# Performance work log

Measured on AMD Instinct MI355X. Metric: run time of the kernel, lower is better.

The kernel has to match this reference:

```python
import jax, jax.numpy as jnp
import numpy as np

N = 50000      # nodes
E = 800000     # edges (before self-loops)
NG = 64        # graphs
H, C = 4, 32   # heads, out channels per head
D = 128        # feature dim == H*C
GS, K = 4, 3   # grid_size, spline_order
NB = GS + K    # number of B-spline bases = 7
NC = 10        # classes
L = 3          # gnn layers

# uniform KAN grid over [-1,1] extended by spline_order on each side
GRID = jnp.arange(-K, GS + K + 1, dtype=jnp.float32) * (2.0 / GS) - 1.0  # [GS+2K+1]


def b_splines(x, grid, k):
    # x: [N, in] -> bases: [N, in, GS+k] via Cox-de Boor recursion
    xe = x[..., None]
    bases = ((xe >= grid[:-1]) & (xe < grid[1:])).astype(x.dtype)
    for p in range(1, k + 1):
        left = (xe - grid[:-(p + 1)]) / (grid[p:-1] - grid[:-(p + 1)]) * bases[..., :-1]
        right = (grid[p + 1:] - xe) / (grid[p + 1:] - grid[1:-p]) * bases[..., 1:]
        bases = left + right
    return bases


def kan_linear(x, base_w, spline_w, scaler):
    # efficient-kan: silu(x)@base_w.T + b_splines(x) contracted with scaled spline weights
    base = jax.nn.silu(x) @ base_w.T
    bs = b_splines(x, GRID, K)                      # [N, in, NB]
    sw = spline_w * scaler[..., None]               # [out, in, NB]
    return base + jnp.einsum('nib,oib->no', bs, sw)


def gat_layer(x, src, dst, base_w, spline_w, scaler, att_src, att_dst, bias):
    n = x.shape[0]
    h = kan_linear(x, base_w, spline_w, scaler).reshape(n, H, C)
    a_src = jnp.sum(h * att_src, axis=-1)           # [N, H]
    a_dst = jnp.sum(h * att_dst, axis=-1)           # [N, H]
    e = jax.nn.leaky_relu(a_src[src] + a_dst[dst], 0.2)  # [Etot, H]
    # segment softmax over incoming edges of each destination node
    m = jax.ops.segment_max(e, dst, num_segments=n)
    ex = jnp.exp(e - m[dst])
    s = jax.ops.segment_sum(ex, dst, num_segments=n)
    alpha = ex / (s[dst] + 1e-16)                   # [Etot, H]
    msg = h[src] * alpha[..., None]                 # [Etot, H, C]
    out = jax.ops.segment_sum(msg, dst, num_segments=n)
    return out.reshape(n, H * C) + bias


def setup_inputs() -> dict:
    key = jax.random.key(0)
    ks = jax.random.split(key, 16)
    inp = {
        'x': jax.random.normal(ks[0], (N, D), dtype=jnp.float32),
        'edge_index': jax.random.randint(ks[1], (2, E), 0, N, dtype=jnp.int32),
        'batch': jnp.sort(jax.random.randint(ks[2], (N,), 0, NG, dtype=jnp.int32)),
        # stacked per-layer GAT+KAN params (all layers are [128 -> 128])
        'base_w': jax.random.normal(ks[3], (L, D, D), dtype=jnp.float32) * 0.05,
        'spline_w': jax.random.normal(ks[4], (L, D, D, NB), dtype=jnp.float32) * 0.05,
        'scaler': jax.random.normal(ks[5], (L, D, D), dtype=jnp.float32) * 0.3 + 1.0,
        'att_src': jax.random.normal(ks[6], (L, H, C), dtype=jnp.float32) * 0.1,
        'att_dst': jax.random.normal(ks[7], (L, H, C), dtype=jnp.float32) * 0.1,
        'bias': jnp.zeros((L, H * C), dtype=jnp.float32),
        # readout KANLinear [128 -> 10]
        'ro_base_w': jax.random.normal(ks[8], (NC, D), dtype=jnp.float32) * 0.05,
        'ro_spline_w': jax.random.normal(ks[9], (NC, D, NB), dtype=jnp.float32) * 0.05,
        'ro_scaler': jax.random.normal(ks[10], (NC, D), dtype=jnp.float32) * 0.3 + 1.0,
    }
    return inp


def reference(x, edge_index, batch, base_w, spline_w, scaler, att_src, att_dst, bias,
              ro_base_w, ro_spline_w, ro_scaler):
    # PyG GATConv default: add self-loops
    loops = jnp.arange(N, dtype=edge_index.dtype)
    src = jnp.concatenate([edge_index[0], loops])
    dst = jnp.concatenate([edge_index[1], loops])
    h = x
    for i in range(L):
        h = gat_layer(h, src, dst, base_w[i], spline_w[i], scaler[i],
                      att_src[i], att_dst[i], bias[i])
        h = jax.nn.silu(h)  # dropout is identity in eval mode
    pooled = jax.ops.segment_sum(h, batch, num_segments=NG)   # global_add_pool [NG, D]
    logits = kan_linear(pooled, ro_base_w, ro_spline_w, ro_scaler)
    return jax.nn.log_softmax(logits, axis=1)
```

## Files before the change

### kernel.cpp

```cpp
#include <hip/hip_runtime.h>
#include <math.h>

#define NN 50000
#define EE 800000
#define ETOT (EE + NN)
#define NGR 64
#define DD 128
#define NCL 10

#define NBUK 128
#define BNODES 391
#define P1CH 3321
#define P2CAP 8704

typedef __attribute__((ext_vector_type(16))) float float16_t;
typedef __attribute__((ext_vector_type(8)))  __bf16 bf16x8;

__device__ __forceinline__ float siluf(float x){ return x / (1.f + __expf(-x)); }

__device__ __forceinline__ unsigned f2bf(float f){
  union { float f; unsigned u; } v; v.f = f;
  unsigned r = v.u + 0x7fffu + ((v.u >> 16) & 1u);
  return (r >> 16) & 0xffffu;
}

__device__ __forceinline__ void kan_feats(float x, float* f8){
  f8[0] = siluf(x);
  float u = 2.f*x + 5.f;
  int cell = -1;
  float n0=0.f,n1=0.f,n2=0.f,n3=0.f;
  if (u >= 0.f && u < 10.f){
    cell = (int)u;
    float t = u - (float)cell;
    float t2 = t*t, t3 = t2*t;
    float omt = 1.f - t;
    const float s6 = 1.f/6.f;
    n0 = t3*s6;
    n1 = s6*(1.f + 3.f*t + 3.f*t2 - 3.f*t3);
    n2 = s6*(4.f - 6.f*t2 + 3.f*t3);
    n3 = omt*omt*omt*s6;
  }
#pragma unroll
  for (int j=0;j<7;++j){
    int k = cell - j;
    float v = (k==0)?n0:((k==1)?n1:((k==2)?n2:((k==3)?n3:0.f)));
    f8[1+j] = v;
  }
}

__device__ __forceinline__ int4 kan_feats_pack(float x){
  unsigned sbf = f2bf(siluf(x));
  float u = 2.f*x + 5.f;
  bool valid = (u >= 0.f) && (u < 10.f);
  float uc = valid ? u : 0.f;
  int cell = (int)uc;
  float t = uc - (float)cell;
  float t2 = t*t, t3 = t2*t, omt = 1.f - t;
  const float s6 = 1.f/6.f;
  float n0 = t3*s6;
  float n1 = s6*(1.f + 3.f*t + 3.f*t2 - 3.f*t3);
  float n2 = s6*(4.f - 6.f*t2 + 3.f*t3);
  float n3 = omt*omt*omt*s6;
  unsigned p0=f2bf(n0), p1=f2bf(n1), p2=f2bf(n2), p3=f2bf(n3);
  unsigned long long P = ((unsigned long long)(p1 | (p0<<16)) << 32)
                       |  (unsigned long long)(p3 | (p2<<16));
  int sh = cell*16 - 48;
  unsigned long long shl    = P << (sh & 63);
  unsigned long long shrhi  = P >> ((64 - sh) & 63);
  unsigned long long shllo2 = P << ((sh - 64) & 63);
  unsigned long long shrlo  = P >> ((-sh) & 63);
  unsigned long long F0, F1;
  if (sh < 0)       { F0 = shrlo; F1 = 0ull; }
  else if (sh < 64) { F0 = shl;   F1 = (sh==0)? 0ull : shrhi; }
  else              { F0 = 0ull;  F1 = shllo2; }
  if (!valid){ F0 = 0ull; F1 = 0ull; }
  unsigned w0 = ((unsigned)(F0 & 0xffffull) << 16) | sbf;
  unsigned w1 = (unsigned)((F0 >> 16) & 0xffffffffull);
  unsigned w2 = (unsigned)((F0 >> 48) & 0xffffull) | (((unsigned)(F1 & 0xffffull)) << 16);
  unsigned w3 = (unsigned)((F1 >> 16) & 0xffffffffull);
  return make_int4((int)w0,(int)w1,(int)w2,(int)w3);
}

__global__ void hist_kernel(const int* __restrict__ ei, int* __restrict__ deg){
  int e = blockIdx.x*256 + threadIdx.x;
  if (e >= ETOT) return;
  int dst = (e < EE) ? ei[EE + e] : (e - EE);
  atomicAdd(&deg[dst], 1);
}

__global__ void scan1_kernel(const int* __restrict__ deg, int* __restrict__ offs, int* __restrict__ part){
  __shared__ int sh[256];
  int tid = threadIdx.x;
  int i = blockIdx.x*256 + tid;
  int v = (i < NN) ? deg[i] : 0;
  sh[tid] = v; __syncthreads();
  for (int o=1;o<256;o<<=1){
    int t2 = (tid >= o) ? sh[tid - o] : 0;
    __syncthreads();
    sh[tid] += t2;
    __syncthreads();
  }
  int incl = sh[tid];
  if (i < NN) offs[i] = incl - v;
  if (tid == 255) part[blockIdx.x] = incl;
}

__global__ void scan2_kernel(int* __restrict__ part, int nb){
  __shared__ int sh[256];
  int tid = threadIdx.x;
  int v = (tid < nb) ? part[tid] : 0;
  sh[tid] = v; __syncthreads();
  for (int o=1;o<256;o<<=1){
    int t2 = (tid >= o) ? sh[tid - o] : 0;
    __syncthreads();
    sh[tid] += t2;
    __syncthreads();
  }
  if (tid < nb) part[tid] = sh[tid] - v;
}

__global__ void scan3_kernel(int* __restrict__ offs, const int* __restrict__ part, int* __restrict__ cursor){
  int i = blockIdx.x*256 + threadIdx.x;
  if (i >= NN) return;
  int o = offs[i] + part[blockIdx.x];
  offs[i] = o;
  cursor[i] = o;
}

__global__ void binit_kernel(const int* __restrict__ offs, int* __restrict__ bcur){
  int b = threadIdx.x;
  if (b < NBUK) bcur[b] = offs[b*BNODES];
}

__global__ __launch_bounds__(256) void binpass_kernel(const int* __restrict__ ei,
                                                      int* __restrict__ bcur,
                                                      unsigned* __restrict__ tmp){
  __shared__ int cnt[NBUK], lexcl[NBUK], gbase[NBUK], lcur[NBUK];
  __shared__ int sc[NBUK];
  __shared__ unsigned entries[P1CH + 7];
  const int t = threadIdx.x;
  const int e0 = blockIdx.x * P1CH;
  int e1 = e0 + P1CH; if (e1 > ETOT) e1 = ETOT;
  const int total = e1 - e0;

  if (t < NBUK){ cnt[t] = 0; lcur[t] = 0; }
  __syncthreads();

  unsigned myE[14]; int myB[14]; int myN = 0;
  for (int e = e0 + t; e < e1; e += 256){
    int src, dst;
    if (e < EE){ src = ei[e]; dst = ei[EE + e]; } else { src = e - EE; dst = src; }
    int b = dst / BNODES;
    int dl = dst - b*BNODES;
    myE[myN] = ((unsigned)b << 25) | ((unsigned)dl << 16) | (unsigned)src;
    myB[myN] = b;
    myN++;
    atomicAdd(&cnt[b], 1);
  }
  __syncthreads();

  if (t < NBUK) sc[t] = cnt[t];
  __syncthreads();
  for (int o=1;o<NBUK;o<<=1){
    int v = 0;
    if (t < NBUK && t >= o) v = sc[t - o];
    __syncthreads();
    if (t < NBUK) sc[t] += v;
    __syncthreads();
  }
  if (t < NBUK) lexcl[t] = sc[t] - cnt[t];
  __syncthreads();

  if (t < NBUK && cnt[t] > 0) gbase[t] = atomicAdd(&bcur[t], cnt[t]);
  __syncthreads();

  for (int k=0;k<myN;++k){
    int b = myB[k];
    int r = lexcl[b] + atomicAdd(&lcur[b], 1);
    entries[r] = myE[k];
  }
  __syncthreads();

  for (int s = t; s < total; s += 256){
    unsigned en = entries[s];
    int b = en >> 25;
    int pos = gbase[b] + (s - lexcl[b]);
    tmp[pos] = en;
  }
}

__global__ __launch_bounds__(256) void scatter_kernel(const unsigned* __restrict__ tmp,
                                                      const int* __restrict__ offs,
                                                      int* __restrict__ cursor,
                                                      int* __restrict__ csr){
  __shared__ unsigned ebuf[P2CAP];
  __shared__ unsigned sbuf[P2CAP];
  __shared__ int dcnt[BNODES+1], dscan[BNODES+1], dcur[BNODES+1];
  __shared__ int sA[512], sB[512];
  const int t = threadIdx.x;
  const int b = blockIdx.x;
  const int lo = b * BNODES;
  const int start = offs[lo];
  const int end = (b < NBUK-1) ? offs[lo + BNODES] : ETOT;
  const int cnt = end - start;

  if (cnt > P2CAP){
    for (int i = t; i < cnt; i += 256){
      unsigned en = tmp[start + i];
      int node = lo + (int)((en >> 16) & 0x1FF);
      int pos = atomicAdd(&cursor[node], 1);
      csr[pos] = (int)(en & 0xFFFF);
    }
    return;
  }

  for (int i = t; i < cnt; i += 256) ebuf[i] = tmp[start + i];
  for (int i = t; i < BNODES+1; i += 256){ dcnt[i] = 0; dcur[i] = 0; }
  __syncthreads();
  for (int i = t; i < cnt; i += 256){
    int dl = (ebuf[i] >> 16) & 0x1FF;
    atomicAdd(&dcnt[dl], 1);
  }
  __syncthreads();

  sA[t]       = (t       < BNODES+1) ? dcnt[t]       : 0;
  sA[t + 256] = (t + 256 < BNODES+1) ? dcnt[t + 256] : 0;
  __syncthreads();
  int* sp = sA; int* dp = sB;
  for (int o=1;o<512;o<<=1){
    dp[t]       = sp[t]       + ((t       >= o) ? sp[t - o]       : 0);
    dp[t + 256] = sp[t + 256] + ((t + 256 >= o) ? sp[t + 256 - o] : 0);
    __syncthreads();
    int* tpp = sp; sp = dp; dp = tpp;
  }
  if (t       < BNODES+1) dscan[t]       = sp[t]       - dcnt[t];
  if (t + 256 < BNODES+1) dscan[t + 256] = sp[t + 256] - dcnt[t + 256];
  __syncthreads();

  for (int i = t; i < cnt; i += 256){
    unsigned en = ebuf[i];
    int dl = (en >> 16) & 0x1FF;
    int r = dscan[dl] + atomicAdd(&dcur[dl], 1);
    sbuf[r] = en & 0xFFFFu;
  }
  __syncthreads();
  for (int i = t; i < cnt; i += 256) csr[start + i] = (int)sbuf[i];
}

__global__ void build_wfrag(const float* __restrict__ bw, const float* __restrict__ sw,
                            const float* __restrict__ sc, unsigned short* __restrict__ wfrag){
  int idx = blockIdx.x*256 + threadIdx.x;
  if (idx >= 3*128*1024) return;
  int k = idx & 1023;
  int o = (idx >> 10) & 127;
  int l = idx >> 17;
  int i = k >> 3, f = k & 7;
  int oi = (l*DD + o)*DD + i;
  float w = (f == 0) ? bw[oi] : sw[oi*7 + (f-1)] * sc[oi];
  int s = k >> 6;
  int sl = (k >> 4) & 3, half = (k >> 3) & 1, j = k & 7;
  int ntile = o >> 5, n = o & 31;
  int dst = l*131072 + s*8192 + (((ntile*4 + sl)*64) + half*32 + n)*8 + j;
  wfrag[dst] = (unsigned short)f2bf(w);
}

__global__ __launch_bounds__(256, 5) void kan_gemm(const float* __restrict__ xin,
                                                const unsigned short* __restrict__ wfrag,
                                                const float* __restrict__ attS,
                                                const float* __restrict__ attD,
                                                unsigned int* __restrict__ hpack,
                                                float* __restrict__ asrc,
                                                float* __restrict__ adst, int layer)
{
  __shared__ __align__(16) unsigned short Afrag[2][4096];
  const int t    = threadIdx.x;
  const int lane = t & 63;
  const int w    = t >> 6;
  const int half = lane >> 5;
  const int mn   = lane & 31;
  const int row0 = blockIdx.x * 32;
  const unsigned short* wl = wfrag + layer*131072;

  const int m_my  = t & 31;
  const int il_my = t >> 5;
  const int grow_my = row0 + m_my;
  const float* xp = xin + (size_t)((grow_my < NN) ? grow_my : 0)*DD + il_my;
  const int fo = (il_my*32 + m_my)*8;

  float xv[16];
#pragma unroll
  for (int s=0;s<16;++s) xv[s] = xp[s*8];

  float16_t acc;
#pragma unroll
  for (int i=0;i<16;++i) acc[i]=0.f;

  int4 Bc[4], Bn[4];
#pragma unroll
  for (int sl=0;sl<4;++sl)
    Bc[sl] = *(const int4*)(wl + ((w*4+sl)*64 + lane)*8);

  *(int4*)(&Afrag[0][fo]) = kan_feats_pack(xv[0]);
  __syncthreads();

  for (int s=0; s<16; ++s){
    if (s < 15){
      const unsigned short* wsrc = wl + (s+1)*8192;
#pragma unroll
      for (int sl=0;sl<4;++sl)
        Bn[sl] = *(const int4*)(wsrc + ((w*4+sl)*64 + lane)*8);
      *(int4*)(&Afrag[(s+1)&1][fo]) = kan_feats_pack(xv[s+1]);
    }
    const unsigned short* A = Afrag[s&1];
#pragma unroll
    for (int sl=0; sl<4; ++sl){
      int4 ai = *(const int4*)(A + (((sl*2 + half)*32) + mn)*8);
      bf16x8 b = __builtin_bit_cast(bf16x8, Bc[sl]);
      acc = __builtin_amdgcn_mfma_f32_32x32x16_bf16(__builtin_bit_cast(bf16x8, ai), b, acc, 0, 0, 0);
    }
#pragma unroll
    for (int sl=0;sl<4;++sl) Bc[sl] = Bn[sl];
    __syncthreads();
  }

  unsigned short* hs = (unsigned short*)Afrag;
#pragma unroll
  for (int reg=0; reg<16; ++reg){
    int row = (reg&3) + 8*(reg>>2) + 4*half;
    hs[row*136 + w*32 + mn] = (unsigned short)f2bf(acc[reg]);
  }
  __syncthreads();
#pragma unroll
  for (int q=0;q<2;++q){
    int p = q*256 + t;
    int row = p >> 4, u4 = p & 15;
    uint4 v = *(const uint4*)((const unsigned int*)(hs + row*136) + u4*4);
    int grow = row0 + row;
    if (grow < NN) *(uint4*)(hpack + (size_t)grow*64 + u4*4) = v;
  }
  if (t < 128){
    int r = t >> 2, h = t & 3;
    const unsigned* hrow = (const unsigned*)(hs + r*136) + h*16;
    const float* ws = attS + (layer*4 + h)*32;
    const float* wd = attD + (layer*4 + h)*32;
    float ss = 0.f, sd = 0.f;
#pragma unroll
    for (int j=0;j<16;++j){
      int jj = (j + r) & 15;
      unsigned u = hrow[jj];
      float flo = __uint_as_float(u << 16);
      float fhi = __uint_as_float(u & 0xffff0000u);
      ss += flo*ws[2*jj] + fhi*ws[2*jj+1];
      sd += flo*wd[2*jj] + fhi*wd[2*jj+1];
    }
    int grow = row0 + r;
    if (grow < NN){ asrc[grow*4 + h] = ss; adst[grow*4 + h] = sd; }
  }
}

__global__ __launch_bounds__(256) void attn_kernel(
    const unsigned int* __restrict__ hpack, const float* __restrict__ asrc, const float* __restrict__ adst,
    const int* __restrict__ offs, const int* __restrict__ deg, const int* __restrict__ csr,
    const float* __restrict__ bias, float* __restrict__ hout, int layer)
{
  const int wave = threadIdx.x >> 6;
  const int lane = threadIdx.x & 63;
  const int n = blockIdx.x*4 + wave;
  if (n >= NN) return;
  const int st = offs[n];
  const int d  = deg[n];
  const int eL = lane >> 2, h = lane & 3;
  const float adh = adst[n*4 + h];

  int   srcv[4];
  float ev[4];
  float mL = -3.4e38f;
#pragma unroll
  for (int c=0;c<4;++c){
    srcv[c] = 0; ev[c] = -3.4e38f;
    int e = c*16 + eL;
    if (e < d){
      int s2 = csr[st + e];
      srcv[c] = s2;
      float e0 = asrc[s2*4 + h] + adh;
      ev[c] = (e0 > 0.f) ? e0 : 0.2f*e0;
      mL = fmaxf(mL, ev[c]);
    }
  }
  for (int c=64; c<d; c+=16){
    int e = c + eL;
    if (e < d){
      int s2 = csr[st + e];
      float e0 = asrc[s2*4 + h] + adh;
      float evv = (e0 > 0.f) ? e0 : 0.2f*e0;
      mL = fmaxf(mL, evv);
    }
  }
#pragma unroll
  for (int o=4;o<64;o<<=1) mL = fmaxf(mL, __shfl_xor(mL, o));

  float av4[4];
  float sL = 0.f;
#pragma unroll
  for (int c=0;c<4;++c){ av4[c] = __expf(ev[c] - mL); sL += av4[c]; }
  for (int c=64; c<d; c+=16){
    int e = c + eL;
    if (e < d){
      int s2 = csr[st + e];
      float e0 = asrc[s2*4 + h] + adh;
      float evv = (e0 > 0.f) ? e0 : 0.2f*e0;
      sL += __expf(evv - mL);
    }
  }
#pragma unroll
  for (int o=4;o<64;o<<=1) sL += __shfl_xor(sL, o);
  const float inv = 1.f/(sL + 1e-16f);

  const int hq = lane >> 4;
  float accL = 0.f, accH = 0.f;
#pragma unroll
  for (int c=0;c<4;++c){
    if (c*16 < d){
      float ac = av4[c] * inv;
      int lim = d - c*16; if (lim > 16) lim = 16;
      unsigned uv[16]; float aj[16];
#pragma unroll
      for (int j=0;j<16;++j){
        int sj = __shfl(srcv[c], j*4);
        aj[j]  = __shfl(ac,      j*4 + hq);
        if (j < lim) uv[j] = hpack[(size_t)sj*64 + lane];
        else         uv[j] = 0u;
      }
#pragma unroll
      for (int j=0;j<16;++j){
        accL = fmaf(aj[j], __uint_as_float(uv[j] << 16),         accL);
        accH = fmaf(aj[j], __uint_as_float(uv[j] & 0xffff0000u), accH);
      }
    }
  }
  for (int c=64; c<d; c+=16){
    int e = c + eL;
    int s2 = 0; float al = 0.f;
    if (e < d){
      s2 = csr[st + e];
      float e0 = asrc[s2*4 + h] + adh;
      float evv = (e0 > 0.f) ? e0 : 0.2f*e0;
      al = __expf(evv - mL) * inv;
    }
    int lim = d - c; if (lim > 16) lim = 16;
    for (int j=0;j<lim;++j){
      int sj = __shfl(s2, j*4);
      float aH = __shfl(al, j*4 + hq);
      unsigned u = hpack[(size_t)sj*64 + lane];
      accL = fmaf(aH, __uint_as_float(u << 16),         accL);
      accH = fmaf(aH, __uint_as_float(u & 0xffff0000u), accH);
    }
  }
  float2 bv = *(const float2*)(bias + layer*DD + 2*lane);
  float o0 = siluf(accL + bv.x);
  float o1 = siluf(accH + bv.y);
  *(float2*)(hout + (size_t)n*DD + 2*lane) = make_float2(o0, o1);
}

__global__ __launch_bounds__(128) void pool_kernel(const float* __restrict__ h,
    const int* __restrict__ batch, float* __restrict__ pooled)
{
  int c = threadIdx.x;
  int n0 = blockIdx.x*128;
  float sum = 0.f; int cur = -1;
  for (int r=0;r<128;++r){
    int n = n0 + r;
    if (n >= NN) break;
    int g = batch[n];
    if (g != cur){
      if (cur >= 0) atomicAdd(&pooled[cur*DD + c], sum);
      cur = g; sum = 0.f;
    }
    sum += h[n*DD + c];
  }
  if (cur >= 0) atomicAdd(&pooled[cur*DD + c], sum);
}

__global__ __launch_bounds__(64) void readout_kernel(const float* __restrict__ pooled,
    const float* __restrict__ bw, const float* __restrict__ sw, const float* __restrict__ sc,
    float* __restrict__ out)
{
  int g = blockIdx.x, lane = threadIdx.x;
  float xa = pooled[g*DD + lane];
  float xb = pooled[g*DD + lane + 64];
  float fa[8], fb[8];
  kan_feats(xa, fa);
  kan_feats(xb, fb);
  float logits[NCL];
#pragma unroll
  for (int c=0;c<NCL;++c){
    int ia = c*DD + lane, ib = ia + 64;
    float sca = sc[ia], scb = sc[ib];
    float p = fa[0]*bw[ia] + fb[0]*bw[ib];
#pragma unroll
    for (int f=1;f<8;++f)
      p += fa[f]*sw[ia*7 + f-1]*sca + fb[f]*sw[ib*7 + f-1]*scb;
#pragma unroll
    for (int o=1;o<64;o<<=1) p += __shfl_xor(p, o);
    logits[c] = p;
  }
  float mx = logits[0];
#pragma unroll
  for (int c=1;c<NCL;++c) mx = fmaxf(mx, logits[c]);
  float lse = 0.f;
#pragma unroll
  for (int c=0;c<NCL;++c) lse += __expf(logits[c]-mx);
  lse = mx + logf(lse);
  if (lane < NCL){
    float v = 0.f;
#pragma unroll
    for (int c=0;c<NCL;++c) if (lane == c) v = logits[c] - lse;
    out[g*NCL + lane] = v;
  }
}

extern "C" void kernel_launch(void* const* d_in, const int* in_sizes, int n_in,
                              void* d_out, int out_size, void* d_ws, size_t ws_size,
                              hipStream_t stream)
{
  const float* x        = (const float*)d_in[0];
  const int*   ei       = (const int*)  d_in[1];
  const int*   batch    = (const int*)  d_in[2];
  const float* base_w   = (const float*)d_in[3];
  const float* spline_w = (const float*)d_in[4];
  const float* scaler   = (const float*)d_in[5];
  const float* att_src  = (const float*)d_in[6];
  const float* att_dst  = (const float*)d_in[7];
  const float* bias     = (const float*)d_in[8];
  const float* ro_bw    = (const float*)d_in[9];
  const float* ro_sw    = (const float*)d_in[10];
  const float* ro_sc    = (const float*)d_in[11];
  float* out = (float*)d_out;

  char* p = (char*)d_ws;
  auto alloc = [&](size_t bytes)->char* {
    char* r = p;
    p += (bytes + 255) & ~(size_t)255;
    return r;
  };
  unsigned int* hpack = (unsigned int*)alloc((size_t)50048*64*4);
  float* hbuf   = (float*)alloc((size_t)NN*DD*4);
  unsigned short* wfrag = (unsigned short*)alloc((size_t)3*131072*2);
  float* asrc   = (float*)alloc((size_t)NN*4*4);
  float* adst   = (float*)alloc((size_t)NN*4*4);
  float* pooled = (float*)alloc((size_t)NGR*DD*4);
  int*   deg    = (int*)alloc((size_t)NN*4);
  int*   offs   = (int*)alloc((size_t)NN*4);
  int*   cursor = (int*)alloc((size_t)NN*4);
  int*   csr    = (int*)alloc((size_t)ETOT*4);
  unsigned* tmp = (unsigned*)alloc((size_t)ETOT*4);
  int*   bcur   = (int*)alloc((size_t)NBUK*4);
  int*   part   = (int*)alloc((size_t)256*4);

  const int nbs = (NN + 255)/256;
  hipMemsetAsync(deg, 0, (size_t)NN*sizeof(int), stream);
  hist_kernel   <<<(ETOT+255)/256, 256, 0, stream>>>(ei, deg);
  scan1_kernel  <<<nbs, 256, 0, stream>>>(deg, offs, part);
  scan2_kernel  <<<1,   256, 0, stream>>>(part, nbs);
  scan3_kernel  <<<nbs, 256, 0, stream>>>(offs, part, cursor);
  binit_kernel  <<<1,   128, 0, stream>>>(offs, bcur);
  binpass_kernel<<<256, 256, 0, stream>>>(ei, bcur, tmp);
  scatter_kernel<<<NBUK,256, 0, stream>>>(tmp, offs, cursor, csr);
  build_wfrag   <<<(3*128*1024)/256, 256, 0, stream>>>(base_w, spline_w, scaler, wfrag);

  const float* cur = x;
  for (int l=0; l<3; ++l){
    kan_gemm   <<<(NN+31)/32, 256, 0, stream>>>(cur, wfrag, att_src, att_dst,
                                                hpack, asrc, adst, l);
    attn_kernel<<<(NN+3)/4,   256, 0, stream>>>(hpack, asrc, adst, offs, deg, csr,
                                                bias, hbuf, l);
    cur = hbuf;
  }
  hipMemsetAsync(pooled, 0, (size_t)NGR*DD*sizeof(float), stream);
  pool_kernel   <<<(NN+127)/128, 128, 0, stream>>>(hbuf, batch, pooled);
  readout_kernel<<<NGR, 64, 0, stream>>>(pooled, ro_bw, ro_sw, ro_sc, out);
}
```

Before: 471.3 us.

## Restructure KAN GEMM so each wave computes a full 32x128 tile from registers

Each wave now owns 32 rows and computes all four 32-column output tiles. A operands are built directly in registers from x via kan_feats_pack, so the shared-memory A staging and the per-step block barriers go away. Blocks now cover 128 rows instead of 32. Weight fragments are read straight from global memory each step without register double-buffering, and the occupancy hint of 5 is dropped. The wave now holds 64 accumulator registers and needs more weight loads per wave, which trades barrier and LDS cost for register pressure and possible occupancy loss.

```diff
diff --git a/kernel.cpp b/kernel.cpp
--- a/kernel.cpp
+++ b/kernel.cpp
@@ -264,7 +264,7 @@
   wfrag[dst] = (unsigned short)f2bf(w);
 }
 
-__global__ __launch_bounds__(256, 5) void kan_gemm(const float* __restrict__ xin,
+__global__ __launch_bounds__(256) void kan_gemm(const float* __restrict__ xin,
                                                 const unsigned short* __restrict__ wfrag,
                                                 const float* __restrict__ attS,
                                                 const float* __restrict__ attD,
@@ -272,77 +272,73 @@
                                                 float* __restrict__ asrc,
                                                 float* __restrict__ adst, int layer)
 {
-  __shared__ __align__(16) unsigned short Afrag[2][4096];
+  __shared__ __align__(16) unsigned short hs4[4][32*136];
   const int t    = threadIdx.x;
   const int lane = t & 63;
-  const int w    = t >> 6;
+  const int wv   = t >> 6;
+  const int m    = lane & 31;
   const int half = lane >> 5;
-  const int mn   = lane & 31;
-  const int row0 = blockIdx.x * 32;
+  const int row0 = blockIdx.x*128 + wv*32;
+  const int grow = row0 + m;
+  const float* xr = xin + (size_t)((grow < NN) ? grow : 0)*DD + half;
   const unsigned short* wl = wfrag + layer*131072;
 
-  const int m_my  = t & 31;
-  const int il_my = t >> 5;
-  const int grow_my = row0 + m_my;
-  const float* xp = xin + (size_t)((grow_my < NN) ? grow_my : 0)*DD + il_my;
-  const int fo = (il_my*32 + m_my)*8;
-
-  float xv[16];
-#pragma unroll
-  for (int s=0;s<16;++s) xv[s] = xp[s*8];
-
-  float16_t acc;
-#pragma unroll
-  for (int i=0;i<16;++i) acc[i]=0.f;
-
-  int4 Bc[4], Bn[4];
-#pragma unroll
-  for (int sl=0;sl<4;++sl)
-    Bc[sl] = *(const int4*)(wl + ((w*4+sl)*64 + lane)*8);
-
-  *(int4*)(&Afrag[0][fo]) = kan_feats_pack(xv[0]);
-  __syncthreads();
-
-  for (int s=0; s<16; ++s){
+  float16_t acc[4];
+#pragma unroll
+  for (int ct=0;ct<4;++ct)
+#pragma unroll
+    for (int i=0;i<16;++i) acc[ct][i]=0.f;
+
+  float xc[4], xn[4];
+#pragma unroll
+  for (int sl=0;sl<4;++sl) xc[sl] = xr[sl*2];
+
+  for (int s=0;s<16;++s){
     if (s < 15){
-      const unsigned short* wsrc = wl + (s+1)*8192;
-#pragma unroll
-      for (int sl=0;sl<4;++sl)
-        Bn[sl] = *(const int4*)(wsrc + ((w*4+sl)*64 + lane)*8);
-      *(int4*)(&Afrag[(s+1)&1][fo]) = kan_feats_pack(xv[s+1]);
-    }
-    const unsigned short* A = Afrag[s&1];
-#pragma unroll
-    for (int sl=0; sl<4; ++sl){
-      int4 ai = *(const int4*)(A + (((sl*2 + half)*32) + mn)*8);
-      bf16x8 b = __builtin_bit_cast(bf16x8, Bc[sl]);
-      acc = __builtin_amdgcn_mfma_f32_32x32x16_bf16(__builtin_bit_cast(bf16x8, ai), b, acc, 0, 0, 0);
-    }
-#pragma unroll
-    for (int sl=0;sl<4;++sl) Bc[sl] = Bn[sl];
-    __syncthreads();
-  }
-
-  unsigned short* hs = (unsigned short*)Afrag;
-#pragma unroll
-  for (int reg=0; reg<16; ++reg){
-    int row = (reg&3) + 8*(reg>>2) + 4*half;
-    hs[row*136 + w*32 + mn] = (unsigned short)f2bf(acc[reg]);
-  }
-  __syncthreads();
+#pragma unroll
+      for (int sl=0;sl<4;++sl) xn[sl] = xr[(s+1)*8 + sl*2];
+    }
+    const unsigned short* ws = wl + s*8192;
+#pragma unroll
+    for (int sl=0;sl<4;++sl){
+      int4 pk = kan_feats_pack(xc[sl]);
+      bf16x8 a = __builtin_bit_cast(bf16x8, pk);
+#pragma unroll
+      for (int ct=0;ct<4;++ct){
+        int4 bi = *(const int4*)(ws + ((ct*4 + sl)*64 + lane)*8);
+        acc[ct] = __builtin_amdgcn_mfma_f32_32x32x16_bf16(a, __builtin_bit_cast(bf16x8, bi), acc[ct], 0, 0, 0);
+      }
+    }
+#pragma unroll
+    for (int sl=0;sl<4;++sl) xc[sl] = xn[sl];
+  }
+
+  unsigned short* hs = hs4[wv];
+#pragma unroll
+  for (int ct=0;ct<4;++ct){
+#pragma unroll
+    for (int reg=0; reg<16; ++reg){
+      int row = (reg&3) + 8*(reg>>2) + 4*half;
+      hs[row*136 + ct*32 + m] = (unsigned short)f2bf(acc[ct][reg]);
+    }
+  }
+  __syncthreads();
+#pragma unroll
+  for (int q=0;q<8;++q){
+    int p = q*64 + lane;
+    int row = p >> 4;
+    int u4 = ((p & 15) + row) & 15;
+    uint4 v = *(const uint4*)((const unsigned int*)(hs + row*136) + u4*4);
+    int gr = row0 + row;
+    if (gr < NN) *(uint4*)(hpack + (size_t)gr*64 + u4*4) = v;
+  }
 #pragma unroll
   for (int q=0;q<2;++q){
-    int p = q*256 + t;
-    int row = p >> 4, u4 = p & 15;
-    uint4 v = *(const uint4*)((const unsigned int*)(hs + row*136) + u4*4);
-    int grow = row0 + row;
-    if (grow < NN) *(uint4*)(hpack + (size_t)grow*64 + u4*4) = v;
-  }
-  if (t < 128){
-    int r = t >> 2, h = t & 3;
+    int p = q*64 + lane;
+    int r = p >> 2, h = p & 3;
     const unsigned* hrow = (const unsigned*)(hs + r*136) + h*16;
-    const float* ws = attS + (layer*4 + h)*32;
-    const float* wd = attD + (layer*4 + h)*32;
+    const float* wsv = attS + (layer*4 + h)*32;
+    const float* wdv = attD + (layer*4 + h)*32;
     float ss = 0.f, sd = 0.f;
 #pragma unroll
     for (int j=0;j<16;++j){
@@ -350,11 +346,11 @@
       unsigned u = hrow[jj];
       float flo = __uint_as_float(u << 16);
       float fhi = __uint_as_float(u & 0xffff0000u);
-      ss += flo*ws[2*jj] + fhi*ws[2*jj+1];
-      sd += flo*wd[2*jj] + fhi*wd[2*jj+1];
-    }
-    int grow = row0 + r;
-    if (grow < NN){ asrc[grow*4 + h] = ss; adst[grow*4 + h] = sd; }
+      ss += flo*wsv[2*jj] + fhi*wsv[2*jj+1];
+      sd += flo*wdv[2*jj] + fhi*wdv[2*jj+1];
+    }
+    int gr = row0 + r;
+    if (gr < NN){ asrc[gr*4 + h] = ss; adst[gr*4 + h] = sd; }
   }
 }
 
@@ -570,8 +566,8 @@
 
   const float* cur = x;
   for (int l=0; l<3; ++l){
-    kan_gemm   <<<(NN+31)/32, 256, 0, stream>>>(cur, wfrag, att_src, att_dst,
-                                                hpack, asrc, adst, l);
+    kan_gemm   <<<(NN+127)/128, 256, 0, stream>>>(cur, wfrag, att_src, att_dst,
+                                                  hpack, asrc, adst, l);
     attn_kernel<<<(NN+3)/4,   256, 0, stream>>>(hpack, asrc, adst, offs, deg, csr,
                                                 bias, hbuf, l);
     cur = hbuf;
```

After: 493.7 us. 1.05x slower.
